# Performance work log

Measured on AMD Instinct MI355X. Metric: run time of the kernel, lower is better.

Reference implementation:

```python
import jax, jax.numpy as jnp
import numpy as np
import math

N, K, M = 4, 2048, 1024   # batch, seq_len, dim_in
DQ, DV = 1024, 1024       # dim_q, dim_v


def _xavier_uniform(k, shape, fan_in, fan_out):
    bound = math.sqrt(6.0 / (fan_in + fan_out))
    return jax.random.uniform(k, shape, jnp.float32, -bound, bound)


def setup_inputs() -> dict:
    key = jax.random.key(0)
    ks = jax.random.split(key, 9)
    query = jax.random.normal(ks[0], (N, K, M), jnp.float32)
    key_t = jax.random.normal(ks[1], (N, K, M), jnp.float32)
    value = jax.random.normal(ks[2], (N, K, M), jnp.float32)
    # causal mask: True above diagonal -> masked out (typical production usage)
    mask = jnp.broadcast_to(jnp.triu(jnp.ones((K, K), bool), k=1), (N, K, K))
    Wq = _xavier_uniform(ks[3], (DQ, M), M, DQ)
    bq = jax.random.uniform(ks[4], (DQ,), jnp.float32, -1 / math.sqrt(M), 1 / math.sqrt(M))
    Wk = _xavier_uniform(ks[5], (DQ, M), M, DQ)
    bk = jax.random.uniform(ks[6], (DQ,), jnp.float32, -1 / math.sqrt(M), 1 / math.sqrt(M))
    Wv = _xavier_uniform(ks[7], (DV, M), M, DV)
    bv = jax.random.uniform(ks[8], (DV,), jnp.float32, -1 / math.sqrt(M), 1 / math.sqrt(M))
    return {"query": query, "key": key_t, "value": value, "mask": mask,
            "Wq": Wq, "bq": bq, "Wk": Wk, "bk": bk, "Wv": Wv, "bv": bv}


def reference(query, key, value, mask, Wq, bq, Wk, bk, Wv, bv):
    # linear projections (torch Linear: x @ W.T + b)
    Q = jnp.einsum("nkm,dm->nkd", query, Wq) + bq   # (N, K, DQ)
    Kp = jnp.einsum("nkm,dm->nkd", key, Wk) + bk    # (N, K, DQ)
    V = jnp.einsum("nkm,dm->nkd", value, Wv) + bv   # (N, K, DV)
    # scaled dot product; scale uses projected dim (dim_q)
    scores = jnp.einsum("nqd,nkd->nqk", Q, Kp) / jnp.sqrt(jnp.float32(DQ))
    scores = jnp.where(mask, jnp.float32(-1e9), scores)
    w = jax.nn.softmax(scores, axis=2)               # (N, K, K)
    y = jnp.einsum("nqk,nkd->nqd", w, V)             # (N, K, DV)
    return y
```

## Files before the change

kernel.cpp:

```cpp
#include <hip/hip_runtime.h>
#include <hip/hip_bf16.h>


typedef __bf16 bf16x8 __attribute__((ext_vector_type(8)));
typedef float  f32x4  __attribute__((ext_vector_type(4)));

#define BM 128
#define BN 128
#define BKK 64

__device__ __forceinline__ int swz(int row, int slot) {
    return row * 128 + (((slot) ^ (row & 7)) << 4);
}

__device__ __forceinline__ void gload16(const __bf16* g, __bf16* l) {
    __builtin_amdgcn_global_load_lds((const __attribute__((address_space(1))) void*)g,
                                     (__attribute__((address_space(3))) void*)l, 16, 0, 0);
}

__device__ __forceinline__ void xcd_remap(int& bx, int& by, int& bz) {
    const int nx = gridDim.x, ny = gridDim.y;
    const int nwg = nx * ny * gridDim.z;
    const int flat = blockIdx.x + nx * (blockIdx.y + ny * blockIdx.z);
    const int q = nwg >> 3, r = nwg & 7;
    const int xcd = flat & 7, idx = flat >> 3;
    const int l = (xcd < r ? xcd * (q + 1) : r * (q + 1) + (xcd - r) * q) + idx;
    bx = l % nx; by = (l / nx) % ny; bz = l / (nx * ny);
}

template<int MODE>
__global__ __launch_bounds__(256)
void gemm_bt(const __bf16* __restrict__ Ap, const __bf16* __restrict__ Bp,
             const float* __restrict__ bias0, const float* __restrict__ bias1,
             const float* __restrict__ bias2, float scaleQ,
             void* __restrict__ Cp, int Kd, int lda, int ldb, int ldc,
             long strideA, long strideB, long strideC)
{
    __shared__ __bf16 smA[2][BM * BKK];
    __shared__ __bf16 smB[2][BN * BKK];

    int bx, by, bz;
    xcd_remap(bx, by, bz);

    const int tid = threadIdx.x;
    const int m0 = by * BM;
    const int n0 = bx * BN;
    if (MODE == 1 && n0 > m0) return;

    const long z = bz;
    int kEnd = Kd;
    if (MODE == 2) { int lim = m0 + BM; kEnd = lim < Kd ? lim : Kd; }

    const int wid = tid >> 6, lane = tid & 63;
    const int wm = (wid >> 1) * 64, wn = (wid & 1) * 64;
    const int g = lane >> 4, li = lane & 15;

    const int rl = lane >> 3;
    const int sg = (lane & 7) ^ rl;
    const __bf16* Az = Ap + z * strideA;
    const __bf16* Bz = Bp + z * strideB;

    f32x4 acc[4][4];
    for (int i = 0; i < 4; i++)
        for (int j = 0; j < 4; j++)
            acc[i][j] = (f32x4){0.f, 0.f, 0.f, 0.f};

    auto STAGE = [&](int buf, int k0) {
        for (int i = 0; i < 4; i++) {
            const int seg = i * 4 + wid;
            const int r = seg * 8 + rl;
            gload16(Az + (long)(m0 + r) * lda + k0 + sg * 8, &smA[buf][seg * 512]);
            gload16(Bz + (long)(n0 + r) * ldb + k0 + sg * 8, &smB[buf][seg * 512]);
        }
    };

    auto COMPUTE = [&](int buf) {
        for (int kk = 0; kk < 2; kk++) {
            const int slot = kk * 4 + g;
            bf16x8 af[4], bfv[4];
            for (int t = 0; t < 4; t++)
                af[t] = *(const bf16x8*)((const char*)&smA[buf][0] + swz(wm + t * 16 + li, slot));
            for (int t = 0; t < 4; t++)
                bfv[t] = *(const bf16x8*)((const char*)&smB[buf][0] + swz(wn + t * 16 + li, slot));
            for (int tm = 0; tm < 4; tm++)
                for (int tn = 0; tn < 4; tn++)
                    acc[tm][tn] = __builtin_amdgcn_mfma_f32_16x16x32_bf16(
                        af[tm], bfv[tn], acc[tm][tn], 0, 0, 0);
        }
    };

    const int nt = kEnd / BKK;
    STAGE(0, 0);
    __syncthreads();
    int cur = 0;
    for (int t = 0; t < nt - 1; ++t) {
        STAGE(cur ^ 1, (t + 1) * BKK);
        COMPUTE(cur);
        __syncthreads();
        cur ^= 1;
    }
    COMPUTE(cur);

    const float scale = (MODE == 0 && z == 0) ? scaleQ : 1.f;
    const float* bias = (MODE == 0) ? (z == 0 ? bias0 : (z == 1 ? bias1 : bias2)) : nullptr;
    for (int tm = 0; tm < 4; tm++) {
        for (int tn = 0; tn < 4; tn++) {
            const int row = m0 + wm + tm * 16 + g * 4;
            const int col = n0 + wn + tn * 16 + li;
            if (MODE == 0) {
                __bf16* C = (__bf16*)Cp + z * strideC;
                const float b = bias[col];
                for (int j = 0; j < 4; j++) {
                    float v = (acc[tm][tn][j] + b) * scale;
                    C[(long)(row + j) * ldc + col] = (__bf16)v;
                }
            } else {
                float* C = (float*)Cp + z * strideC;
                for (int j = 0; j < 4; j++)
                    C[(long)(row + j) * ldc + col] = acc[tm][tn][j];
            }
        }
    }
}

__global__ __launch_bounds__(256)
void cvt3(const float* __restrict__ s0, const float* __restrict__ s1,
          const float* __restrict__ s2, __bf16* __restrict__ d0,
          __bf16* __restrict__ d1, __bf16* __restrict__ d2, long n)
{
    const int zz = blockIdx.y;
    const float* src = zz == 0 ? s0 : (zz == 1 ? s1 : s2);
    __bf16* dst = zz == 0 ? d0 : (zz == 1 ? d1 : d2);
    long i = ((long)blockIdx.x * 256 + threadIdx.x) * 8;
    const long stride = (long)gridDim.x * 2048;
    for (; i < n; i += stride) {
        float4 a = *(const float4*)(src + i);
        float4 b = *(const float4*)(src + i + 4);
        bf16x8 v;
        v[0] = (__bf16)a.x; v[1] = (__bf16)a.y; v[2] = (__bf16)a.z; v[3] = (__bf16)a.w;
        v[4] = (__bf16)b.x; v[5] = (__bf16)b.y; v[6] = (__bf16)b.z; v[7] = (__bf16)b.w;
        *(bf16x8*)(dst + i) = v;
    }
}

__global__ __launch_bounds__(256)
void transpose2d(const ushort* __restrict__ V, ushort* __restrict__ Vt)
{
    __shared__ ushort t[64][65];
    const int d0 = blockIdx.x * 64, k0 = blockIdx.y * 64;
    const long nb = blockIdx.z;
    const ushort* Vb = V + nb * 2048 * 1024;
    ushort* Vtb = Vt + nb * 1024 * 2048;

    for (int i = 0; i < 16; i++) {
        int lin = threadIdx.x + 256 * i;
        int r = lin >> 6, c = lin & 63;
        t[r][c] = Vb[(long)(k0 + r) * 1024 + d0 + c];
    }
    __syncthreads();
    for (int i = 0; i < 16; i++) {
        int lin = threadIdx.x + 256 * i;
        int r = lin >> 6, c = lin & 63;
        Vtb[(long)(d0 + r) * 2048 + k0 + c] = t[c][r];
    }
}

__global__ __launch_bounds__(256)
void softmax_causal(float* __restrict__ S)
{
    const int q = blockIdx.x;
    const long rowoff = (long)blockIdx.y * 2048 + q;
    const float* Srow = S + rowoff * 2048;
    __bf16* Prow = (__bf16*)S + rowoff * 4096;

    const int tid = threadIdx.x;
    const int wid = tid >> 6, lane = tid & 63;

    float v[8];
    float mx = -1e30f;
    for (int i = 0; i < 8; i++) {
        int idx = tid + 256 * i;
        v[i] = (idx <= q) ? Srow[idx] : -1e30f;
        mx = fmaxf(mx, v[i]);
    }
    for (int off = 32; off; off >>= 1) mx = fmaxf(mx, __shfl_xor(mx, off));
    __shared__ float red[8];
    if (lane == 0) red[wid] = mx;
    __syncthreads();
    mx = fmaxf(fmaxf(red[0], red[1]), fmaxf(red[2], red[3]));

    float e[8];
    float s = 0.f;
    for (int i = 0; i < 8; i++) {
        int idx = tid + 256 * i;
        e[i] = (idx <= q) ? __expf(v[i] - mx) : 0.f;
        s += e[i];
    }
    for (int off = 32; off; off >>= 1) s += __shfl_xor(s, off);
    if (lane == 0) red[4 + wid] = s;
    __syncthreads();
    s = red[4] + red[5] + red[6] + red[7];
    const float inv = 1.f / s;

    for (int i = 0; i < 8; i++)
        Prow[tid + 256 * i] = (__bf16)(e[i] * inv);
}

extern "C" void kernel_launch(void* const* d_in, const int* in_sizes, int n_in,
                              void* d_out, int out_size, void* d_ws, size_t ws_size,
                              hipStream_t stream) {
    const float* query = (const float*)d_in[0];
    const float* key   = (const float*)d_in[1];
    const float* value = (const float*)d_in[2];
    const float* Wq = (const float*)d_in[4];
    const float* bq = (const float*)d_in[5];
    const float* Wk = (const float*)d_in[6];
    const float* bk = (const float*)d_in[7];
    const float* Wv = (const float*)d_in[8];
    const float* bv = (const float*)d_in[9];
    float* out = (float*)d_out;

    char* ws = (char*)d_ws;
    const long MB = 1L << 20;
    __bf16* QKV = (__bf16*)(ws);
    __bf16* Vp  = QKV + 2 * 8388608L;
    __bf16* Vt  = (__bf16*)(ws + 48 * MB);
    float*  S   = (float*) (ws + 64 * MB);
    __bf16* Xb  = (__bf16*)(ws + 64 * MB);
    __bf16* Wb  = (__bf16*)(ws + 112 * MB);

    const dim3 blk(256);
    const long nX = 2048L * 1024 * 4;
    const long nW = 1024L * 1024;

    cvt3<<<dim3(1024, 3), blk, 0, stream>>>(query, key, value,
        Xb, Xb + 8388608L, Xb + 2 * 8388608L, nX);
    cvt3<<<dim3(512, 3), blk, 0, stream>>>(Wq, Wk, Wv,
        Wb, Wb + 1048576L, Wb + 2 * 1048576L, nW);

    gemm_bt<0><<<dim3(8, 64, 3), blk, 0, stream>>>(Xb, Wb, bq, bk, bv, 1.f / 32.f,
        QKV, 1024, 1024, 1024, 1024, 8388608L, 1048576L, 8388608L);

    transpose2d<<<dim3(16, 32, 4), blk, 0, stream>>>((const ushort*)Vp, (ushort*)Vt);

    gemm_bt<1><<<dim3(16, 16, 4), blk, 0, stream>>>(QKV, QKV + 8388608L,
        nullptr, nullptr, nullptr, 1.f, S,
        1024, 1024, 1024, 2048, 2048L * 1024, 2048L * 1024, 2048L * 2048);

    softmax_causal<<<dim3(2048, 4), blk, 0, stream>>>(S);

    gemm_bt<2><<<dim3(8, 16, 4), blk, 0, stream>>>((__bf16*)S, Vt,
        nullptr, nullptr, nullptr, 1.f, out,
        2048, 4096, 2048, 1024, 2048L * 4096, 1024L * 2048, 2048L * 1024);
}
```

Measured before the change: 195.7 us.

## Use 256x256-tile, 8-wave pipelined GEMM for the QKV projection

Replaces the 128x128-tile projection GEMM with a dedicated 512-thread kernel using 256x256 tiles, double-buffered direct-to-LDS loads with explicit vmcnt waits, and a four-phase ping-pong MFMA schedule with barriers and setprio. Larger tiles raise arithmetic intensity per LDS and global load, and the phased schedule is meant to overlap fragment loads with MFMA work. The grid shrinks to 384 workgroups, which may leave some CUs under-occupied, and LDS use per block rises to 128KB. The bias/scale path is removed from the generic gemm_bt.

After: 212.4 us. 8.5% more time.

```diff
diff --git a/kernel.cpp b/kernel.cpp
--- a/kernel.cpp
+++ b/kernel.cpp
@@ -28,11 +28,137 @@
     bx = l % nx; by = (l / nx) % ny; bz = l / (nx * ny);
 }
 
+template<int MH, int NH, bool DOA, bool DOB>
+__device__ __forceinline__ void phase256(const char* LAb, const char* LBb,
+    int wM, int wn, int g, int li,
+    bf16x8 (&aF)[4][2], bf16x8 (&bF)[2][2], f32x4 (&acc)[8][4])
+{
+    if (DOA) {
+#pragma unroll
+        for (int i = 0; i < 4; i++)
+#pragma unroll
+            for (int kk = 0; kk < 2; kk++) {
+                const int row = wM * 128 + MH * 64 + i * 16 + li;
+                aF[i][kk] = *(const bf16x8*)(LAb + swz(row, kk * 4 + g));
+            }
+    }
+    if (DOB) {
+#pragma unroll
+        for (int j = 0; j < 2; j++)
+#pragma unroll
+            for (int kk = 0; kk < 2; kk++) {
+                const int row = wn * 64 + NH * 32 + j * 16 + li;
+                bF[j][kk] = *(const bf16x8*)(LBb + swz(row, kk * 4 + g));
+            }
+    }
+    __builtin_amdgcn_s_barrier();
+    __builtin_amdgcn_sched_barrier(0);
+    __builtin_amdgcn_s_setprio(1);
+#pragma unroll
+    for (int kk = 0; kk < 2; kk++)
+#pragma unroll
+        for (int i = 0; i < 4; i++)
+#pragma unroll
+            for (int j = 0; j < 2; j++)
+                acc[MH * 4 + i][NH * 2 + j] = __builtin_amdgcn_mfma_f32_16x16x32_bf16(
+                    aF[i][kk], bF[j][kk], acc[MH * 4 + i][NH * 2 + j], 0, 0, 0);
+    __builtin_amdgcn_s_setprio(0);
+    __builtin_amdgcn_s_barrier();
+    __builtin_amdgcn_sched_barrier(0);
+}
+
+__global__ __launch_bounds__(512)
+void gemm256_proj(const __bf16* __restrict__ Ap, const __bf16* __restrict__ Bp,
+                  const float* __restrict__ b0, const float* __restrict__ b1,
+                  const float* __restrict__ b2, float scaleQ, __bf16* __restrict__ Cp)
+{
+    __shared__ __bf16 LA[2][256 * 64];
+    __shared__ __bf16 LB[2][256 * 64];
+
+    int bx, by, bz;
+    xcd_remap(bx, by, bz);
+    const int m0 = by * 256, n0 = bx * 256;
+    const long z = bz;
+
+    const int tid = threadIdx.x;
+    const int wid = tid >> 6, lane = tid & 63;
+    const int wM = wid >> 2;
+    const int wn = wid & 3;
+    const int g = lane >> 4, li = lane & 15;
+    const int rl = lane >> 3;
+    const int sg = (lane & 7) ^ rl;
+
+    const __bf16* Az = Ap + z * 8388608L;
+    const __bf16* Bz = Bp + z * 1048576L;
+
+    auto ISSUE = [&](int buf, int k0) {
+#pragma unroll
+        for (int i = 0; i < 4; i++) {
+            const int seg = wid * 4 + i;
+            const int r = seg * 8 + rl;
+            gload16(Az + (long)(m0 + r) * 1024 + k0 + sg * 8, &LA[buf][seg * 512]);
+        }
+#pragma unroll
+        for (int i = 0; i < 4; i++) {
+            const int seg = wid * 4 + i;
+            const int r = seg * 8 + rl;
+            gload16(Bz + (long)(n0 + r) * 1024 + k0 + sg * 8, &LB[buf][seg * 512]);
+        }
+    };
+
+    f32x4 acc[8][4];
+#pragma unroll
+    for (int i = 0; i < 8; i++)
+#pragma unroll
+        for (int j = 0; j < 4; j++)
+            acc[i][j] = (f32x4){0.f, 0.f, 0.f, 0.f};
+    bf16x8 aF[4][2], bF[2][2];
+
+    const int nt = 16;
+    ISSUE(0, 0);
+    int cur = 0;
+    for (int t = 0; t < nt; ++t) {
+        if (t + 1 < nt) {
+            ISSUE(cur ^ 1, (t + 1) * 64);
+            __builtin_amdgcn_sched_barrier(0);
+            asm volatile("s_waitcnt vmcnt(8)" ::: "memory");
+        } else {
+            __builtin_amdgcn_sched_barrier(0);
+            asm volatile("s_waitcnt vmcnt(0)" ::: "memory");
+        }
+        __builtin_amdgcn_sched_barrier(0);
+        __builtin_amdgcn_s_barrier();
+        __builtin_amdgcn_sched_barrier(0);
+
+        const char* LAb = (const char*)&LA[cur][0];
+        const char* LBb = (const char*)&LB[cur][0];
+        phase256<0, 0, true,  true >(LAb, LBb, wM, wn, g, li, aF, bF, acc);
+        phase256<0, 1, false, true >(LAb, LBb, wM, wn, g, li, aF, bF, acc);
+        phase256<1, 1, true,  false>(LAb, LBb, wM, wn, g, li, aF, bF, acc);
+        phase256<1, 0, false, true >(LAb, LBb, wM, wn, g, li, aF, bF, acc);
+        cur ^= 1;
+    }
+
+    const float scale = (z == 0) ? scaleQ : 1.f;
+    const float* bias = z == 0 ? b0 : (z == 1 ? b1 : b2);
+    __bf16* C = Cp + z * 8388608L;
+#pragma unroll
+    for (int fi = 0; fi < 8; fi++) {
+#pragma unroll
+        for (int fj = 0; fj < 4; fj++) {
+            const int row = m0 + wM * 128 + fi * 16 + g * 4;
+            const int col = n0 + wn * 64 + fj * 16 + li;
+            const float b = bias[col];
+#pragma unroll
+            for (int jj = 0; jj < 4; jj++)
+                C[(long)(row + jj) * 1024 + col] = (__bf16)((acc[fi][fj][jj] + b) * scale);
+        }
+    }
+}
+
 template<int MODE>
 __global__ __launch_bounds__(256)
 void gemm_bt(const __bf16* __restrict__ Ap, const __bf16* __restrict__ Bp,
-             const float* __restrict__ bias0, const float* __restrict__ bias1,
-             const float* __restrict__ bias2, float scaleQ,
              void* __restrict__ Cp, int Kd, int lda, int ldb, int ldc,
              long strideA, long strideB, long strideC)
 {
@@ -54,7 +180,6 @@
     const int wid = tid >> 6, lane = tid & 63;
     const int wm = (wid >> 1) * 64, wn = (wid & 1) * 64;
     const int g = lane >> 4, li = lane & 15;
-
     const int rl = lane >> 3;
     const int sg = (lane & 7) ^ rl;
     const __bf16* Az = Ap + z * strideA;
@@ -101,24 +226,13 @@
     }
     COMPUTE(cur);
 
-    const float scale = (MODE == 0 && z == 0) ? scaleQ : 1.f;
-    const float* bias = (MODE == 0) ? (z == 0 ? bias0 : (z == 1 ? bias1 : bias2)) : nullptr;
     for (int tm = 0; tm < 4; tm++) {
         for (int tn = 0; tn < 4; tn++) {
             const int row = m0 + wm + tm * 16 + g * 4;
             const int col = n0 + wn + tn * 16 + li;
-            if (MODE == 0) {
-                __bf16* C = (__bf16*)Cp + z * strideC;
-                const float b = bias[col];
-                for (int j = 0; j < 4; j++) {
-                    float v = (acc[tm][tn][j] + b) * scale;
-                    C[(long)(row + j) * ldc + col] = (__bf16)v;
-                }
-            } else {
-                float* C = (float*)Cp + z * strideC;
-                for (int j = 0; j < 4; j++)
-                    C[(long)(row + j) * ldc + col] = acc[tm][tn][j];
-            }
+            float* C = (float*)Cp + z * strideC;
+            for (int j = 0; j < 4; j++)
+                C[(long)(row + j) * ldc + col] = acc[tm][tn][j];
         }
     }
 }
@@ -238,18 +352,16 @@
     cvt3<<<dim3(512, 3), blk, 0, stream>>>(Wq, Wk, Wv,
         Wb, Wb + 1048576L, Wb + 2 * 1048576L, nW);
 
-    gemm_bt<0><<<dim3(8, 64, 3), blk, 0, stream>>>(Xb, Wb, bq, bk, bv, 1.f / 32.f,
-        QKV, 1024, 1024, 1024, 1024, 8388608L, 1048576L, 8388608L);
+    gemm256_proj<<<dim3(4, 32, 3), dim3(512), 0, stream>>>(
+        Xb, Wb, bq, bk, bv, 1.f / 32.f, QKV);
 
     transpose2d<<<dim3(16, 32, 4), blk, 0, stream>>>((const ushort*)Vp, (ushort*)Vt);
 
-    gemm_bt<1><<<dim3(16, 16, 4), blk, 0, stream>>>(QKV, QKV + 8388608L,
-        nullptr, nullptr, nullptr, 1.f, S,
+    gemm_bt<1><<<dim3(16, 16, 4), blk, 0, stream>>>(QKV, QKV + 8388608L, S,
         1024, 1024, 1024, 2048, 2048L * 1024, 2048L * 1024, 2048L * 2048);
 
     softmax_causal<<<dim3(2048, 4), blk, 0, stream>>>(S);
 
-    gemm_bt<2><<<dim3(8, 16, 4), blk, 0, stream>>>((__bf16*)S, Vt,
-        nullptr, nullptr, nullptr, 1.f, out,
+    gemm_bt<2><<<dim3(8, 16, 4), blk, 0, stream>>>((__bf16*)S, Vt, out,
         2048, 4096, 2048, 1024, 2048L * 4096, 1024L * 2048, 2048L * 1024);
 }
```

## Fuse fp32-to-bf16 input conversion and V transpose into projection GEMM

Applied to the files above, without the earlier changes.

The projection GEMM now reads the fp32 activations directly, converts them to bf16 in registers and writes them into swizzled LDS. This removes the separate activation conversion kernel and its bf16 round trip through memory. For the V projection the epilogue transposes the tile through LDS and writes Vt directly, which removes the standalone transpose kernel. Softmax also stops writing probabilities beyond the causal block boundary that the PV GEMM never reads. The cost is register-staged A loads that are less asynchronous than direct global-to-LDS loads, plus higher register pressure.

New measurement: 183.8 us. 6.1% less time.

```diff
diff --git a/kernel.cpp b/kernel.cpp
--- a/kernel.cpp
+++ b/kernel.cpp
@@ -28,11 +28,154 @@
     bx = l % nx; by = (l / nx) % ny; bz = l / (nx * ny);
 }
 
+__global__ __launch_bounds__(256)
+void gemm_proj(const float* __restrict__ xq, const float* __restrict__ xk,
+               const float* __restrict__ xv, const __bf16* __restrict__ Wb,
+               const float* __restrict__ b0, const float* __restrict__ b1,
+               const float* __restrict__ b2, float scaleQ,
+               __bf16* __restrict__ QKV, __bf16* __restrict__ Vt)
+{
+    __shared__ char smem[65536];
+    __bf16* smA = (__bf16*)smem;
+    __bf16* smB = (__bf16*)(smem + 32768);
+
+    int bx, by, bz;
+    xcd_remap(bx, by, bz);
+    const int m0 = by * BM, n0 = bx * BN;
+    const int z = bz;
+    const float* X = z == 0 ? xq : (z == 1 ? xk : xv);
+    const __bf16* Bz = Wb + (long)z * 1048576L;
+
+    const int tid = threadIdx.x;
+    const int wid = tid >> 6, lane = tid & 63;
+    const int wm = (wid >> 1) * 64, wn = (wid & 1) * 64;
+    const int g = lane >> 4, li = lane & 15;
+    const int rl = lane >> 3;
+    const int sl = lane & 7;
+    const int sg = sl ^ rl;
+
+    float4 aReg[4][2];
+    auto ISSUE_A = [&](int k0) {
+#pragma unroll
+        for (int i = 0; i < 4; i++) {
+            const int r = (i * 4 + wid) * 8 + rl;
+            const float* p = X + (long)(m0 + r) * 1024 + k0 + sl * 8;
+            aReg[i][0] = *(const float4*)p;
+            aReg[i][1] = *(const float4*)(p + 4);
+        }
+    };
+    auto WRITE_A = [&](int buf) {
+        char* base = (char*)(smA + buf * 8192);
+#pragma unroll
+        for (int i = 0; i < 4; i++) {
+            const int r = (i * 4 + wid) * 8 + rl;
+            bf16x8 v;
+            v[0] = (__bf16)aReg[i][0].x; v[1] = (__bf16)aReg[i][0].y;
+            v[2] = (__bf16)aReg[i][0].z; v[3] = (__bf16)aReg[i][0].w;
+            v[4] = (__bf16)aReg[i][1].x; v[5] = (__bf16)aReg[i][1].y;
+            v[6] = (__bf16)aReg[i][1].z; v[7] = (__bf16)aReg[i][1].w;
+            *(bf16x8*)(base + swz(r, sl)) = v;
+        }
+    };
+    auto STAGE_B = [&](int buf, int k0) {
+#pragma unroll
+        for (int i = 0; i < 4; i++) {
+            const int seg = i * 4 + wid;
+            const int r = seg * 8 + rl;
+            gload16(Bz + (long)(n0 + r) * 1024 + k0 + sg * 8, smB + buf * 8192 + seg * 512);
+        }
+    };
+
+    f32x4 acc[4][4];
+#pragma unroll
+    for (int i = 0; i < 4; i++)
+#pragma unroll
+        for (int j = 0; j < 4; j++)
+            acc[i][j] = (f32x4){0.f, 0.f, 0.f, 0.f};
+
+    auto COMPUTE = [&](int buf) {
+        const char* bA = (const char*)(smA + buf * 8192);
+        const char* bB = (const char*)(smB + buf * 8192);
+#pragma unroll
+        for (int kk = 0; kk < 2; kk++) {
+            const int slot = kk * 4 + g;
+            bf16x8 af[4], bfv[4];
+#pragma unroll
+            for (int t = 0; t < 4; t++)
+                af[t] = *(const bf16x8*)(bA + swz(wm + t * 16 + li, slot));
+#pragma unroll
+            for (int t = 0; t < 4; t++)
+                bfv[t] = *(const bf16x8*)(bB + swz(wn + t * 16 + li, slot));
+#pragma unroll
+            for (int tm = 0; tm < 4; tm++)
+#pragma unroll
+                for (int tn = 0; tn < 4; tn++)
+                    acc[tm][tn] = __builtin_amdgcn_mfma_f32_16x16x32_bf16(
+                        af[tm], bfv[tn], acc[tm][tn], 0, 0, 0);
+        }
+    };
+
+    const int nt = 16;
+    ISSUE_A(0); STAGE_B(0, 0); WRITE_A(0);
+    __syncthreads();
+    int cur = 0;
+    for (int t = 0; t < nt - 1; ++t) {
+        ISSUE_A((t + 1) * BKK);
+        STAGE_B(cur ^ 1, (t + 1) * BKK);
+        COMPUTE(cur);
+        WRITE_A(cur ^ 1);
+        __syncthreads();
+        cur ^= 1;
+    }
+    COMPUTE(cur);
+
+    if (z < 2) {
+        const float scale = (z == 0) ? scaleQ : 1.f;
+        const float* bias = (z == 0) ? b0 : b1;
+        __bf16* C = QKV + (long)z * 8388608L;
+#pragma unroll
+        for (int tm = 0; tm < 4; tm++)
+#pragma unroll
+            for (int tn = 0; tn < 4; tn++) {
+                const int row = m0 + wm + tm * 16 + g * 4;
+                const int col = n0 + wn + tn * 16 + li;
+                const float b = bias[col];
+#pragma unroll
+                for (int j = 0; j < 4; j++)
+                    C[(long)(row + j) * 1024 + col] = (__bf16)((acc[tm][tn][j] + b) * scale);
+            }
+    } else {
+        __syncthreads();
+        __bf16* T = (__bf16*)smem;
+#pragma unroll
+        for (int tm = 0; tm < 4; tm++)
+#pragma unroll
+            for (int tn = 0; tn < 4; tn++) {
+                const int rowl = wm + tm * 16 + g * 4;
+                const int coll = wn + tn * 16 + li;
+                const float b = b2[n0 + coll];
+#pragma unroll
+                for (int j = 0; j < 4; j++)
+                    T[coll * 136 + rowl + j] = (__bf16)(acc[tm][tn][j] + b);
+            }
+        __syncthreads();
+        const long nb = m0 >> 11;
+        const int kbase = m0 & 2047;
+        __bf16* Vtb = Vt + nb * 2097152L;
+#pragma unroll
+        for (int it = 0; it < 8; it++) {
+            const int lin = tid + 256 * it;
+            const int c = lin >> 4;
+            const int r0 = (lin & 15) * 8;
+            bf16x8 v = *(const bf16x8*)(T + c * 136 + r0);
+            *(bf16x8*)(Vtb + (long)(n0 + c) * 2048 + kbase + r0) = v;
+        }
+    }
+}
+
 template<int MODE>
 __global__ __launch_bounds__(256)
 void gemm_bt(const __bf16* __restrict__ Ap, const __bf16* __restrict__ Bp,
-             const float* __restrict__ bias0, const float* __restrict__ bias1,
-             const float* __restrict__ bias2, float scaleQ,
              void* __restrict__ Cp, int Kd, int lda, int ldb, int ldc,
              long strideA, long strideB, long strideC)
 {
@@ -54,7 +197,6 @@
     const int wid = tid >> 6, lane = tid & 63;
     const int wm = (wid >> 1) * 64, wn = (wid & 1) * 64;
     const int g = lane >> 4, li = lane & 15;
-
     const int rl = lane >> 3;
     const int sg = (lane & 7) ^ rl;
     const __bf16* Az = Ap + z * strideA;
@@ -101,24 +243,13 @@
     }
     COMPUTE(cur);
 
-    const float scale = (MODE == 0 && z == 0) ? scaleQ : 1.f;
-    const float* bias = (MODE == 0) ? (z == 0 ? bias0 : (z == 1 ? bias1 : bias2)) : nullptr;
     for (int tm = 0; tm < 4; tm++) {
         for (int tn = 0; tn < 4; tn++) {
             const int row = m0 + wm + tm * 16 + g * 4;
             const int col = n0 + wn + tn * 16 + li;
-            if (MODE == 0) {
-                __bf16* C = (__bf16*)Cp + z * strideC;
-                const float b = bias[col];
-                for (int j = 0; j < 4; j++) {
-                    float v = (acc[tm][tn][j] + b) * scale;
-                    C[(long)(row + j) * ldc + col] = (__bf16)v;
-                }
-            } else {
-                float* C = (float*)Cp + z * strideC;
-                for (int j = 0; j < 4; j++)
-                    C[(long)(row + j) * ldc + col] = acc[tm][tn][j];
-            }
+            float* C = (float*)Cp + z * strideC;
+            for (int j = 0; j < 4; j++)
+                C[(long)(row + j) * ldc + col] = acc[tm][tn][j];
         }
     }
 }
@@ -144,28 +275,6 @@
 }
 
 __global__ __launch_bounds__(256)
-void transpose2d(const ushort* __restrict__ V, ushort* __restrict__ Vt)
-{
-    __shared__ ushort t[64][65];
-    const int d0 = blockIdx.x * 64, k0 = blockIdx.y * 64;
-    const long nb = blockIdx.z;
-    const ushort* Vb = V + nb * 2048 * 1024;
-    ushort* Vtb = Vt + nb * 1024 * 2048;
-
-    for (int i = 0; i < 16; i++) {
-        int lin = threadIdx.x + 256 * i;
-        int r = lin >> 6, c = lin & 63;
-        t[r][c] = Vb[(long)(k0 + r) * 1024 + d0 + c];
-    }
-    __syncthreads();
-    for (int i = 0; i < 16; i++) {
-        int lin = threadIdx.x + 256 * i;
-        int r = lin >> 6, c = lin & 63;
-        Vtb[(long)(d0 + r) * 2048 + k0 + c] = t[c][r];
-    }
-}
-
-__global__ __launch_bounds__(256)
 void softmax_causal(float* __restrict__ S)
 {
     const int q = blockIdx.x;
@@ -202,8 +311,11 @@
     s = red[4] + red[5] + red[6] + red[7];
     const float inv = 1.f / s;
 
-    for (int i = 0; i < 8; i++)
-        Prow[tid + 256 * i] = (__bf16)(e[i] * inv);
+    const int qc = q | 127;
+    for (int i = 0; i < 8; i++) {
+        int idx = tid + 256 * i;
+        if (idx <= qc) Prow[idx] = (__bf16)(e[i] * inv);
+    }
 }
 
 extern "C" void kernel_launch(void* const* d_in, const int* in_sizes, int n_in,
@@ -223,33 +335,24 @@
     char* ws = (char*)d_ws;
     const long MB = 1L << 20;
     __bf16* QKV = (__bf16*)(ws);
-    __bf16* Vp  = QKV + 2 * 8388608L;
     __bf16* Vt  = (__bf16*)(ws + 48 * MB);
     float*  S   = (float*) (ws + 64 * MB);
-    __bf16* Xb  = (__bf16*)(ws + 64 * MB);
     __bf16* Wb  = (__bf16*)(ws + 112 * MB);
 
     const dim3 blk(256);
-    const long nX = 2048L * 1024 * 4;
     const long nW = 1024L * 1024;
 
-    cvt3<<<dim3(1024, 3), blk, 0, stream>>>(query, key, value,
-        Xb, Xb + 8388608L, Xb + 2 * 8388608L, nX);
     cvt3<<<dim3(512, 3), blk, 0, stream>>>(Wq, Wk, Wv,
         Wb, Wb + 1048576L, Wb + 2 * 1048576L, nW);
 
-    gemm_bt<0><<<dim3(8, 64, 3), blk, 0, stream>>>(Xb, Wb, bq, bk, bv, 1.f / 32.f,
-        QKV, 1024, 1024, 1024, 1024, 8388608L, 1048576L, 8388608L);
-
-    transpose2d<<<dim3(16, 32, 4), blk, 0, stream>>>((const ushort*)Vp, (ushort*)Vt);
-
-    gemm_bt<1><<<dim3(16, 16, 4), blk, 0, stream>>>(QKV, QKV + 8388608L,
-        nullptr, nullptr, nullptr, 1.f, S,
+    gemm_proj<<<dim3(8, 64, 3), blk, 0, stream>>>(
+        query, key, value, Wb, bq, bk, bv, 1.f / 32.f, QKV, Vt);
+
+    gemm_bt<1><<<dim3(16, 16, 4), blk, 0, stream>>>(QKV, QKV + 8388608L, S,
         1024, 1024, 1024, 2048, 2048L * 1024, 2048L * 1024, 2048L * 2048);
 
     softmax_causal<<<dim3(2048, 4), blk, 0, stream>>>(S);
 
-    gemm_bt<2><<<dim3(8, 16, 4), blk, 0, stream>>>((__bf16*)S, Vt,
-        nullptr, nullptr, nullptr, 1.f, out,
+    gemm_bt<2><<<dim3(8, 16, 4), blk, 0, stream>>>((__bf16*)S, Vt, out,
         2048, 4096, 2048, 1024, 2048L * 4096, 1024L * 2048, 2048L * 1024);
 }
```
